# Optimization experiments

Measured on AMD Instinct MI355X. Metric: run time of the kernel, lower is better.

Reference implementation:

```python
import jax, jax.numpy as jnp
import numpy as np

B, CK, CV, T, H, W = 2, 64, 256, 8, 48, 48

def setup_inputs() -> dict:
    key = jax.random.key(0)
    k1, k2, k3, k4, k5, k6 = jax.random.split(key, 6)
    return {
        "query_key": jax.random.normal(k1, (B, CK, H, W), jnp.float32),
        "query_selection": jax.random.uniform(k2, (B, CK, H, W), jnp.float32),
        "memory_key": jax.random.normal(k3, (B, CK, T, H, W), jnp.float32),
        "memory_shrinkage": jax.random.uniform(k4, (B, 1, T, H, W), jnp.float32),
        "msk_value": jax.random.normal(k5, (B, 1, CV, T, H, W), jnp.float32),
        "uncert_prob": jax.random.uniform(k6, (B, 1, H, W), jnp.float32),
    }

def reference(query_key, query_selection, memory_key, memory_shrinkage, msk_value, uncert_prob):
    b, ck, h, w = query_key.shape
    t = memory_key.shape[2]
    hw = h * w
    thw = t * hw
    num_obj, cv = msk_value.shape[1], msk_value.shape[2]

    mk = memory_key.reshape(b, ck, thw)            # B,CK,THW
    ms = memory_shrinkage.reshape(b, thw, 1)       # B,THW,1
    qk = query_key.reshape(b, ck, hw)              # B,CK,HW
    qe = query_selection.reshape(b, ck, hw)        # B,CK,HW

    # L2 similarity with selection weighting: -(mk - qk)^2 weighted by qe per channel
    a_sq = jnp.einsum('bct,bcn->btn', mk * mk, qe)          # B,THW,HW
    two_ab = 2.0 * jnp.einsum('bct,bcn->btn', mk, qk * qe)  # B,THW,HW
    b_sq = jnp.sum(qe * qk * qk, axis=1, keepdims=True)     # B,1,HW
    similarity = (-a_sq + two_ab - b_sq) * ms / jnp.sqrt(jnp.float32(ck))

    # softmax over the memory (THW) axis
    affinity = jax.nn.softmax(similarity, axis=1)           # B,THW,HW

    # weighted readout of memory values
    mv = msk_value.reshape(b, num_obj * cv, thw)            # B,CV,THW
    pixel_readout = jnp.einsum('bct,btn->bcn', mv, affinity)
    pixel_readout = pixel_readout.reshape(b, num_obj, cv, h, w)

    # uncertainty-weighted blend with last memory frame's value
    last_val = msk_value[:, :, :, -1]                       # B,no,CV,H,W
    p = uncert_prob[:, None]                                # B,1,1,H,W
    blended = pixel_readout * p + last_val[:, None, 0] * (1.0 - p) if False else pixel_readout * p + last_val * (1.0 - p)
    return blended
```

## Files before the change

kernel.cpp:

```cpp
#include <hip/hip_runtime.h>
#include <math.h>

#define NB 2
#define CKD 64
#define CVD 256
#define TD 8
#define HWD 2304
#define THWD 18432
#define QB 64
#define NQB (HWD / QB)
#define KVT 32

typedef __bf16 bf16_t;
typedef __bf16 bf16x8 __attribute__((ext_vector_type(8)));
typedef __bf16 bf16x4 __attribute__((ext_vector_type(4)));
typedef float f32x4 __attribute__((ext_vector_type(4)));
typedef unsigned int u32;

__device__ __forceinline__ void gload16(const void* g, void* l) {
    __builtin_amdgcn_global_load_lds((const __attribute__((address_space(1))) u32*)g,
                                     (__attribute__((address_space(3))) u32*)l, 16, 0, 0);
}

__global__ void prep_kf(const float* __restrict__ mk, char* __restrict__ KF2) {
    __shared__ float tile[64][65];
    const int b = blockIdx.y;
    const int kv0 = blockIdx.x * 64;
    const int tid = threadIdx.x;
    {
        const int c = tid >> 2, seg = tid & 3;
        const float* src = mk + ((size_t)b * CKD + c) * THWD + kv0;
#pragma unroll
        for (int j = 0; j < 4; ++j) {
            int ch = seg + j * 4;
            f32x4 v = *(const f32x4*)(src + ch * 4);
#pragma unroll
            for (int x = 0; x < 4; ++x) tile[c][ch * 4 + x] = v[x];
        }
    }
    __syncthreads();
#pragma unroll
    for (int k = 0; k < 4; ++k) {
        int gid = k * 256 + tid;
        int kvl = gid >> 4, G = gid & 15;
        bf16x8 o;
#pragma unroll
        for (int e = 0; e < 8; ++e) {
            int c = G * 8 + e;
            float v;
            if (c < 64) v = tile[c][kvl];
            else { float m = tile[c - 64][kvl]; v = m * m; }
            o[e] = (bf16_t)v;
        }
        size_t byte = (((size_t)b * 1152 + ((kv0 + kvl) >> 4)) * 16 + (kvl & 15)) * 256 +
                      (size_t)((G ^ (kvl & 7)) << 4);
        *(bf16x8*)(KF2 + byte) = o;
    }
}

__global__ void prep_qf(const float* __restrict__ qk, const float* __restrict__ qe,
                        char* __restrict__ QF2, float* __restrict__ bsq) {
    __shared__ float tk[64][65];
    __shared__ float te[64][65];
    __shared__ float bs[4][64];
    const int b = blockIdx.y;
    const int q0 = blockIdx.x * 64;
    const int tid = threadIdx.x;
    {
        const int c = tid >> 2, seg = tid & 3;
        const float* s1 = qk + ((size_t)b * CKD + c) * HWD + q0;
        const float* s2 = qe + ((size_t)b * CKD + c) * HWD + q0;
#pragma unroll
        for (int j = 0; j < 4; ++j) {
            int ch = seg + j * 4;
            f32x4 v1 = *(const f32x4*)(s1 + ch * 4);
            f32x4 v2 = *(const f32x4*)(s2 + ch * 4);
#pragma unroll
            for (int x = 0; x < 4; ++x) { tk[c][ch * 4 + x] = v1[x]; te[c][ch * 4 + x] = v2[x]; }
        }
    }
    __syncthreads();
    {
        int qls = tid & 63, cp = tid >> 6;
        float s = 0.f;
#pragma unroll
        for (int cc = 0; cc < 16; ++cc) {
            int c = cp * 16 + cc;
            float kk = tk[c][qls];
            s = fmaf(te[c][qls] * kk, kk, s);
        }
        bs[cp][qls] = s;
    }
#pragma unroll
    for (int k = 0; k < 4; ++k) {
        int gid = k * 256 + tid;
        int qll = gid >> 4, G = gid & 15;
        int ks = G >> 2, G2 = G & 3;
        bf16x8 o;
#pragma unroll
        for (int e = 0; e < 8; ++e) {
            int c = G * 8 + e;
            float v;
            if (c < 64) v = 2.f * tk[c][qll] * te[c][qll];
            else v = -te[c - 64][qll];
            o[e] = (bf16_t)v;
        }
        size_t byte = ((((size_t)b * 144 + blockIdx.x * 4 + (qll >> 4)) * 4 + ks) * 16 +
                       (qll & 15)) * 64 + (size_t)(G2 << 4);
        *(bf16x8*)(QF2 + byte) = o;
    }
    __syncthreads();
    if (tid < 64) bsq[b * HWD + q0 + tid] = bs[0][tid] + bs[1][tid] + bs[2][tid] + bs[3][tid];
}

__global__ void mv_t(const float* __restrict__ mv, char* __restrict__ mvT) {
    __shared__ float tile[64][65];
    const int b = blockIdx.z;
    const int cv0 = blockIdx.y * 64;
    const int kv0 = blockIdx.x * 64;
    const int tid = threadIdx.x;
    {
        const int cvl = tid >> 2, seg = tid & 3;
        const float* src = mv + ((size_t)b * CVD + cv0 + cvl) * THWD + kv0;
#pragma unroll
        for (int j = 0; j < 4; ++j) {
            int ch = seg + j * 4;
            f32x4 v = *(const f32x4*)(src + ch * 4);
#pragma unroll
            for (int x = 0; x < 4; ++x) tile[cvl][ch * 4 + x] = v[x];
        }
    }
    __syncthreads();
#pragma unroll
    for (int k = 0; k < 2; ++k) {
        int gid = k * 256 + tid;
        int cvl = gid >> 3, gseg = gid & 7;
        int t32l = gseg >> 2, G = gseg & 3;
        int cv = cv0 + cvl;
        bf16x8 o;
#pragma unroll
        for (int e = 0; e < 8; ++e) o[e] = (bf16_t)tile[cvl][gseg * 8 + e];
        size_t byte = (((size_t)b * 576 + (kv0 >> 5) + t32l) * 256 + cv) * 64 +
                      (size_t)((G ^ ((cv >> 1) & 3)) << 4);
        *(bf16x8*)(mvT + byte) = o;
    }
}

__global__ __launch_bounds__(256, 3) void fused(
    const char* __restrict__ KF2, const char* __restrict__ QF2,
    const char* __restrict__ mvT, const float* __restrict__ ms,
    const float* __restrict__ bsq, float* __restrict__ accP,
    float* __restrict__ lP, int split, int tiles) {
    __shared__ __align__(16) char kf_s[2][8192];
    __shared__ __align__(16) char mv_s[2][16384];
    __shared__ __align__(16) char w_s[4096];
    __shared__ float l_s[2][64];

    const int tid = threadIdx.x;
    const int lane = tid & 63;
    const int wave = tid >> 6;
    const int wq = wave & 1;
    const int wc = wave >> 1;
    const int r = lane & 15;
    const int g = lane >> 4;
    const int swq = (r >> 1) & 3;

    const int nwg = gridDim.x;
    const int bid = blockIdx.x;
    const int id = (bid & 7) * (nwg >> 3) + (bid >> 3);
    const int sp = id / 72;
    const int rem = id - sp * 72;
    const int b = rem / 36;
    const int qblk = rem - b * 36;

    const int tbase = sp * (THWD / split);

    const char* KFb = KF2 + (size_t)b * THWD * 256;
    const char* QFb = QF2 + (size_t)b * 144 * 4096;
    const char* mvTb = mvT + (size_t)b * 576 * 16384;
    const float* msb = ms + (size_t)b * THWD;

    bf16x8 qf[2][4];
    float bsqr[2];
#pragma unroll
    for (int ql = 0; ql < 2; ++ql) {
        int qb16 = qblk * 4 + wq * 2 + ql;
#pragma unroll
        for (int ks = 0; ks < 4; ++ks)
            qf[ql][ks] = *(const bf16x8*)(QFb + ((size_t)qb16 * 4 + ks) * 1024 + r * 64 + g * 16);
        bsqr[ql] = bsq[b * HWD + qblk * 64 + wq * 32 + ql * 16 + r];
    }

    f32x4 acc[8][2];
#pragma unroll
    for (int i = 0; i < 8; ++i)
#pragma unroll
        for (int j = 0; j < 2; ++j) acc[i][j] = (f32x4){0.f, 0.f, 0.f, 0.f};
    float lacc[2] = {0.f, 0.f};

    auto stage = [&](int buf, int t0) {
        const char* gk = KFb + (size_t)(t0 >> 4) * 4096 + wave * 2048 + lane * 16;
        char* lk = &kf_s[buf][wave * 2048];
        gload16(gk, lk);
        gload16(gk + 1024, lk + 1024);
        const char* gm = mvTb + (size_t)(t0 >> 5) * 16384 + wave * 4096 + lane * 16;
        char* lm = &mv_s[buf][wave * 4096];
#pragma unroll
        for (int i = 0; i < 4; ++i) gload16(gm + i * 1024, lm + i * 1024);
    };

    f32x4 msv[2];
    stage(0, tbase);
    msv[0] = *(const f32x4*)(msb + tbase + wc * 16 + g * 4);

#pragma unroll 2
    for (int it = 0; it < tiles; ++it) {
        const int t0 = tbase + it * KVT;
        const char* kf_c = kf_s[it & 1];
        const char* mv_c = mv_s[it & 1];

        asm volatile("s_waitcnt vmcnt(0) lgkmcnt(0)" ::: "memory");
        __builtin_amdgcn_s_barrier();

        if (it + 1 < tiles) {
            stage((it + 1) & 1, t0 + KVT);
            msv[(it + 1) & 1] = *(const f32x4*)(msb + t0 + KVT + wc * 16 + g * 4);
        }

        f32x4 S[2];
        S[0] = (f32x4){0.f, 0.f, 0.f, 0.f};
        S[1] = (f32x4){0.f, 0.f, 0.f, 0.f};
#pragma unroll
        for (int ks = 0; ks < 4; ++ks) {
            bf16x8 kff = *(const bf16x8*)(kf_c + (wc * 16 + r) * 256 +
                                          (((ks * 4 + g) ^ (r & 7)) << 4));
#pragma unroll
            for (int ql = 0; ql < 2; ++ql)
                S[ql] = __builtin_amdgcn_mfma_f32_16x16x32_bf16(kff, qf[ql][ks], S[ql], 0, 0, 0);
        }

        f32x4 msc = msv[it & 1];
#pragma unroll
        for (int ql = 0; ql < 2; ++ql) {
            int q = wq * 32 + ql * 16 + r;
            f32x4 sv = S[ql];
            float w0 = __expf((sv[0] - bsqr[ql]) * (msc[0] * 0.125f));
            float w1 = __expf((sv[1] - bsqr[ql]) * (msc[1] * 0.125f));
            float w2 = __expf((sv[2] - bsqr[ql]) * (msc[2] * 0.125f));
            float w3 = __expf((sv[3] - bsqr[ql]) * (msc[3] * 0.125f));
            lacc[ql] += (w0 + w1) + (w2 + w3);
            bf16x4 wb;
            wb[0] = (bf16_t)w0; wb[1] = (bf16_t)w1; wb[2] = (bf16_t)w2; wb[3] = (bf16_t)w3;
            *(bf16x4*)(&w_s[q * 64 + (((wc * 2 + (g >> 1)) ^ swq) << 4) + (g & 1) * 8]) = wb;
        }
        asm volatile("s_waitcnt lgkmcnt(0)" ::: "memory");
        __builtin_amdgcn_s_barrier();

        bf16x8 wf[2];
#pragma unroll
        for (int ql = 0; ql < 2; ++ql) {
            int q = wq * 32 + ql * 16 + r;
            wf[ql] = *(const bf16x8*)(&w_s[q * 64 + ((g ^ swq) << 4)]);
        }
#pragma unroll
        for (int cvt = 0; cvt < 8; ++cvt) {
            bf16x8 mvf = *(const bf16x8*)(mv_c + (wc * 128 + cvt * 16 + r) * 64 +
                                          ((g ^ swq) << 4));
#pragma unroll
            for (int ql = 0; ql < 2; ++ql)
                acc[cvt][ql] = __builtin_amdgcn_mfma_f32_16x16x32_bf16(mvf, wf[ql], acc[cvt][ql], 0, 0, 0);
        }
    }

    size_t pb = (size_t)(b * NQB + qblk) * split + sp;
    float* accB = accP + pb * (CVD * QB);
#pragma unroll
    for (int cvt = 0; cvt < 8; ++cvt)
#pragma unroll
        for (int ql = 0; ql < 2; ++ql) {
            int q = wq * 32 + ql * 16 + r;
#pragma unroll
            for (int i = 0; i < 4; ++i)
                accB[(size_t)(wc * 128 + cvt * 16 + g * 4 + i) * QB + q] = acc[cvt][ql][i];
        }
#pragma unroll
    for (int ql = 0; ql < 2; ++ql) {
        float v = lacc[ql];
        v += __shfl_xor(v, 16);
        v += __shfl_xor(v, 32);
        if (lane < 16) l_s[wc][wq * 32 + ql * 16 + lane] = v;
    }
    __syncthreads();
    if (tid < QB) lP[pb * QB + tid] = l_s[0][tid] + l_s[1][tid];
}

__global__ void combine(const float* __restrict__ accP, const float* __restrict__ lP,
                        const float* __restrict__ mv, const float* __restrict__ up,
                        float* __restrict__ out, int split) {
    int idx = blockIdx.x * 256 + threadIdx.x;
    if (idx >= NB * CVD * HWD) return;
    int n = idx % HWD;
    int cv = (idx / HWD) % CVD;
    int b = idx / (HWD * CVD);
    int qblk = n / QB, nl = n % QB;
    size_t base = ((size_t)(b * NQB + qblk) * split) * (CVD * QB) + (size_t)cv * QB + nl;
    size_t lbase = ((size_t)(b * NQB + qblk) * split) * QB + nl;
    float a = 0.f, l = 0.f;
    for (int s = 0; s < split; ++s) {
        a += accP[base + (size_t)s * (CVD * QB)];
        l += lP[lbase + (size_t)s * QB];
    }
    float ro = a / l;
    float p = up[b * HWD + n];
    float last = mv[((size_t)b * CVD + cv) * THWD + (TD - 1) * HWD + n];
    out[idx] = ro * p + last * (1.f - p);
}

extern "C" void kernel_launch(void* const* d_in, const int* in_sizes, int n_in,
                              void* d_out, int out_size, void* d_ws,
                              size_t ws_size, hipStream_t stream) {
    const float* qk = (const float*)d_in[0];
    const float* qe = (const float*)d_in[1];
    const float* mk = (const float*)d_in[2];
    const float* ms = (const float*)d_in[3];
    const float* mv = (const float*)d_in[4];
    const float* up = (const float*)d_in[5];
    float* out = (float*)d_out;

    char* ws = (char*)d_ws;
    size_t off = 0;
    auto alloc = [&](size_t bytes) {
        size_t o = off;
        off += (bytes + 255) & ~(size_t)255;
        return o;
    };
    size_t kf_o = alloc((size_t)NB * THWD * 256);
    size_t qf_o = alloc((size_t)NB * 144 * 4096);
    size_t mvt_o = alloc((size_t)NB * 576 * 16384);
    size_t bsq_o = alloc((size_t)NB * HWD * 4);
    size_t fixed = off;

    int split = 16;
    while (split > 1) {
        size_t need = fixed +
                      (((size_t)NB * NQB * split * CVD * QB * 4 + 255) & ~(size_t)255) +
                      (((size_t)NB * NQB * split * QB * 4 + 255) & ~(size_t)255);
        if (need <= ws_size) break;
        split >>= 1;
    }
    size_t lp_o = alloc((size_t)NB * NQB * split * QB * 4);
    size_t acc_o = alloc((size_t)NB * NQB * split * CVD * QB * 4);

    char* KF2 = ws + kf_o;
    char* QF2 = ws + qf_o;
    char* MVT = ws + mvt_o;
    float* bsqp = (float*)(ws + bsq_o);
    float* lPp = (float*)(ws + lp_o);
    float* accPp = (float*)(ws + acc_o);

    int tiles = (THWD / split) / KVT;

    prep_kf<<<dim3(THWD / 64, NB), 256, 0, stream>>>(mk, KF2);
    prep_qf<<<dim3(HWD / 64, NB), 256, 0, stream>>>(qk, qe, QF2, bsqp);
    mv_t<<<dim3(THWD / 64, CVD / 64, NB), 256, 0, stream>>>(mv, MVT);

    int nwg = NB * NQB * split;
    fused<<<nwg, 256, 0, stream>>>(KF2, QF2, MVT, ms, bsqp, accPp, lPp, split, tiles);

    combine<<<((size_t)NB * CVD * HWD + 255) / 256, 256, 0, stream>>>(accPp, lPp, mv,
                                                                      up, out, split);
}
```

Measured before the change: 163.3 us.

## Restructure fused attention tiles: smaller query block, larger KV tile, direct value loads

Shrinks the query block from 64 to 32 and doubles the KV tile to 64, fixing the split at 8. Each wave now handles a 16-row KV slice: two waves split the channel halves and the two KV halves are reduced in-block through LDS. Value fragments are loaded straight from global memory into registers instead of being staged through LDS, and the mv_t layout drops its swizzle to match. The combine kernel is vectorised to four channels per thread. Together these change data reuse, LDS traffic and grid size, at the cost of more global value reads per block and an extra in-block reduction.

```diff
diff --git a/kernel.cpp b/kernel.cpp
--- a/kernel.cpp
+++ b/kernel.cpp
@@ -7,9 +7,11 @@
 #define TD 8
 #define HWD 2304
 #define THWD 18432
-#define QB 64
+#define QB 32
 #define NQB (HWD / QB)
-#define KVT 32
+#define KVT 64
+#define SPLIT 8
+#define TILES (THWD / SPLIT / KVT)
 
 typedef __bf16 bf16_t;
 typedef __bf16 bf16x8 __attribute__((ext_vector_type(8)));
@@ -46,13 +48,13 @@
         bf16x8 o;
 #pragma unroll
         for (int e = 0; e < 8; ++e) {
-            int c = G * 8 + e;
+            int ch = G * 8 + e;
             float v;
-            if (c < 64) v = tile[c][kvl];
-            else { float m = tile[c - 64][kvl]; v = m * m; }
+            if (ch < 64) v = tile[ch][kvl];
+            else { float m = tile[ch - 64][kvl]; v = m * m; }
             o[e] = (bf16_t)v;
         }
-        size_t byte = (((size_t)b * 1152 + ((kv0 + kvl) >> 4)) * 16 + (kvl & 15)) * 256 +
+        size_t byte = (((size_t)b * (THWD / 16) + ((kv0 + kvl) >> 4)) * 16 + (kvl & 15)) * 256 +
                       (size_t)((G ^ (kvl & 7)) << 4);
         *(bf16x8*)(KF2 + byte) = o;
     }
@@ -85,9 +87,9 @@
         float s = 0.f;
 #pragma unroll
         for (int cc = 0; cc < 16; ++cc) {
-            int c = cp * 16 + cc;
-            float kk = tk[c][qls];
-            s = fmaf(te[c][qls] * kk, kk, s);
+            int ch = cp * 16 + cc;
+            float kk = tk[ch][qls];
+            s = fmaf(te[ch][qls] * kk, kk, s);
         }
         bs[cp][qls] = s;
     }
@@ -99,13 +101,13 @@
         bf16x8 o;
 #pragma unroll
         for (int e = 0; e < 8; ++e) {
-            int c = G * 8 + e;
+            int ch = G * 8 + e;
             float v;
-            if (c < 64) v = 2.f * tk[c][qll] * te[c][qll];
-            else v = -te[c - 64][qll];
+            if (ch < 64) v = 2.f * tk[ch][qll] * te[ch][qll];
+            else v = -te[ch - 64][qll];
             o[e] = (bf16_t)v;
         }
-        size_t byte = ((((size_t)b * 144 + blockIdx.x * 4 + (qll >> 4)) * 4 + ks) * 16 +
+        size_t byte = ((((size_t)b * (HWD / 16) + blockIdx.x * 4 + (qll >> 4)) * 4 + ks) * 16 +
                        (qll & 15)) * 64 + (size_t)(G2 << 4);
         *(bf16x8*)(QF2 + byte) = o;
     }
@@ -136,12 +138,12 @@
         int gid = k * 256 + tid;
         int cvl = gid >> 3, gseg = gid & 7;
         int t32l = gseg >> 2, G = gseg & 3;
-        int cv = cv0 + cvl;
         bf16x8 o;
 #pragma unroll
-        for (int e = 0; e < 8; ++e) o[e] = (bf16_t)tile[cvl][gseg * 8 + e];
-        size_t byte = (((size_t)b * 576 + (kv0 >> 5) + t32l) * 256 + cv) * 64 +
-                      (size_t)((G ^ ((cv >> 1) & 3)) << 4);
+        for (int e = 0; e < 8; ++e)
+            o[e] = (bf16_t)tile[cvl][t32l * 32 + (e >> 2) * 16 + G * 4 + (e & 3)];
+        size_t byte = (((size_t)b * (THWD / 32) + (kv0 >> 5) + t32l) * 256 + cv0 + cvl) * 64 +
+                      (size_t)(G << 4);
         *(bf16x8*)(mvT + byte) = o;
     }
 }
@@ -150,45 +152,42 @@
     const char* __restrict__ KF2, const char* __restrict__ QF2,
     const char* __restrict__ mvT, const float* __restrict__ ms,
     const float* __restrict__ bsq, float* __restrict__ accP,
-    float* __restrict__ lP, int split, int tiles) {
-    __shared__ __align__(16) char kf_s[2][8192];
-    __shared__ __align__(16) char mv_s[2][16384];
-    __shared__ __align__(16) char w_s[4096];
-    __shared__ float l_s[2][64];
+    float* __restrict__ lP) {
+    __shared__ __align__(16) char kf_s[2][16384];
+    __shared__ __align__(16) char w_lds[4096];
+    __shared__ float l_s[4][QB];
 
     const int tid = threadIdx.x;
     const int lane = tid & 63;
     const int wave = tid >> 6;
-    const int wq = wave & 1;
-    const int wc = wave >> 1;
+    const int s = wave >> 1;
+    const int c = wave & 1;
+    const int st = s * 2 + c;
     const int r = lane & 15;
     const int g = lane >> 4;
-    const int swq = (r >> 1) & 3;
-
-    const int nwg = gridDim.x;
+
     const int bid = blockIdx.x;
-    const int id = (bid & 7) * (nwg >> 3) + (bid >> 3);
-    const int sp = id / 72;
-    const int rem = id - sp * 72;
-    const int b = rem / 36;
-    const int qblk = rem - b * 36;
-
-    const int tbase = sp * (THWD / split);
+    const int id = (bid & 7) * (NB * NQB) + (bid >> 3);
+    const int sp = id / (NB * NQB);
+    const int rem = id % (NB * NQB);
+    const int b = rem / NQB;
+    const int qblk = rem % NQB;
+    const int tbase = sp * (THWD / SPLIT);
 
     const char* KFb = KF2 + (size_t)b * THWD * 256;
-    const char* QFb = QF2 + (size_t)b * 144 * 4096;
-    const char* mvTb = mvT + (size_t)b * 576 * 16384;
+    const char* QFb = QF2 + (size_t)b * (HWD / 16) * 4096;
+    const char* mvTb = mvT + (size_t)b * (THWD / 32) * 16384;
     const float* msb = ms + (size_t)b * THWD;
 
     bf16x8 qf[2][4];
     float bsqr[2];
 #pragma unroll
     for (int ql = 0; ql < 2; ++ql) {
-        int qb16 = qblk * 4 + wq * 2 + ql;
+        int qb16 = qblk * 2 + ql;
 #pragma unroll
         for (int ks = 0; ks < 4; ++ks)
             qf[ql][ks] = *(const bf16x8*)(QFb + ((size_t)qb16 * 4 + ks) * 1024 + r * 64 + g * 16);
-        bsqr[ql] = bsq[b * HWD + qblk * 64 + wq * 32 + ql * 16 + r];
+        bsqr[ql] = bsq[b * HWD + qblk * QB + ql * 16 + r];
     }
 
     f32x4 acc[8][2];
@@ -199,50 +198,44 @@
     float lacc[2] = {0.f, 0.f};
 
     auto stage = [&](int buf, int t0) {
-        const char* gk = KFb + (size_t)(t0 >> 4) * 4096 + wave * 2048 + lane * 16;
-        char* lk = &kf_s[buf][wave * 2048];
-        gload16(gk, lk);
-        gload16(gk + 1024, lk + 1024);
-        const char* gm = mvTb + (size_t)(t0 >> 5) * 16384 + wave * 4096 + lane * 16;
-        char* lm = &mv_s[buf][wave * 4096];
-#pragma unroll
-        for (int i = 0; i < 4; ++i) gload16(gm + i * 1024, lm + i * 1024);
+        const char* gk = KFb + (size_t)t0 * 256 + wave * 4096 + lane * 16;
+        char* lk = &kf_s[buf][wave * 4096];
+#pragma unroll
+        for (int i = 0; i < 4; ++i) gload16(gk + i * 1024, lk + i * 1024);
     };
-
-    f32x4 msv[2];
     stage(0, tbase);
-    msv[0] = *(const f32x4*)(msb + tbase + wc * 16 + g * 4);
 
 #pragma unroll 2
-    for (int it = 0; it < tiles; ++it) {
+    for (int it = 0; it < TILES; ++it) {
         const int t0 = tbase + it * KVT;
         const char* kf_c = kf_s[it & 1];
-        const char* mv_c = mv_s[it & 1];
 
         asm volatile("s_waitcnt vmcnt(0) lgkmcnt(0)" ::: "memory");
         __builtin_amdgcn_s_barrier();
 
-        if (it + 1 < tiles) {
-            stage((it + 1) & 1, t0 + KVT);
-            msv[(it + 1) & 1] = *(const f32x4*)(msb + t0 + KVT + wc * 16 + g * 4);
-        }
+        bf16x8 mvf[8];
+#pragma unroll
+        for (int cvt = 0; cvt < 8; ++cvt)
+            mvf[cvt] = *(const bf16x8*)(mvTb +
+                ((size_t)((t0 >> 5) + s) * 256 + c * 128 + cvt * 16 + r) * 64 + g * 16);
+        f32x4 msc = *(const f32x4*)(msb + t0 + st * 16 + g * 4);
+
+        if (it + 1 < TILES) stage((it + 1) & 1, t0 + KVT);
 
         f32x4 S[2];
         S[0] = (f32x4){0.f, 0.f, 0.f, 0.f};
         S[1] = (f32x4){0.f, 0.f, 0.f, 0.f};
 #pragma unroll
         for (int ks = 0; ks < 4; ++ks) {
-            bf16x8 kff = *(const bf16x8*)(kf_c + (wc * 16 + r) * 256 +
+            bf16x8 kff = *(const bf16x8*)(kf_c + (st * 16 + r) * 256 +
                                           (((ks * 4 + g) ^ (r & 7)) << 4));
 #pragma unroll
             for (int ql = 0; ql < 2; ++ql)
                 S[ql] = __builtin_amdgcn_mfma_f32_16x16x32_bf16(kff, qf[ql][ks], S[ql], 0, 0, 0);
         }
 
-        f32x4 msc = msv[it & 1];
 #pragma unroll
         for (int ql = 0; ql < 2; ++ql) {
-            int q = wq * 32 + ql * 16 + r;
             f32x4 sv = S[ql];
             float w0 = __expf((sv[0] - bsqr[ql]) * (msc[0] * 0.125f));
             float w1 = __expf((sv[1] - bsqr[ql]) * (msc[1] * 0.125f));
@@ -251,69 +244,86 @@
             lacc[ql] += (w0 + w1) + (w2 + w3);
             bf16x4 wb;
             wb[0] = (bf16_t)w0; wb[1] = (bf16_t)w1; wb[2] = (bf16_t)w2; wb[3] = (bf16_t)w3;
-            *(bf16x4*)(&w_s[q * 64 + (((wc * 2 + (g >> 1)) ^ swq) << 4) + (g & 1) * 8]) = wb;
+            *(bf16x4*)(&w_lds[((s * 32 + ql * 16 + r) * 4 + g) * 16 + c * 8]) = wb;
         }
         asm volatile("s_waitcnt lgkmcnt(0)" ::: "memory");
         __builtin_amdgcn_s_barrier();
 
         bf16x8 wf[2];
 #pragma unroll
-        for (int ql = 0; ql < 2; ++ql) {
-            int q = wq * 32 + ql * 16 + r;
-            wf[ql] = *(const bf16x8*)(&w_s[q * 64 + ((g ^ swq) << 4)]);
-        }
-#pragma unroll
-        for (int cvt = 0; cvt < 8; ++cvt) {
-            bf16x8 mvf = *(const bf16x8*)(mv_c + (wc * 128 + cvt * 16 + r) * 64 +
-                                          ((g ^ swq) << 4));
+        for (int ql = 0; ql < 2; ++ql)
+            wf[ql] = *(const bf16x8*)(&w_lds[((s * 32 + ql * 16 + r) * 4 + g) * 16]);
+#pragma unroll
+        for (int cvt = 0; cvt < 8; ++cvt)
 #pragma unroll
             for (int ql = 0; ql < 2; ++ql)
-                acc[cvt][ql] = __builtin_amdgcn_mfma_f32_16x16x32_bf16(mvf, wf[ql], acc[cvt][ql], 0, 0, 0);
-        }
-    }
-
-    size_t pb = (size_t)(b * NQB + qblk) * split + sp;
-    float* accB = accP + pb * (CVD * QB);
-#pragma unroll
-    for (int cvt = 0; cvt < 8; ++cvt)
-#pragma unroll
-        for (int ql = 0; ql < 2; ++ql) {
-            int q = wq * 32 + ql * 16 + r;
-#pragma unroll
-            for (int i = 0; i < 4; ++i)
-                accB[(size_t)(wc * 128 + cvt * 16 + g * 4 + i) * QB + q] = acc[cvt][ql][i];
-        }
+                acc[cvt][ql] = __builtin_amdgcn_mfma_f32_16x16x32_bf16(
+                    mvf[cvt], wf[ql], acc[cvt][ql], 0, 0, 0);
+    }
+
+    __syncthreads();
+    float* red = (float*)&kf_s[0][0];
+    if (s == 1) {
+#pragma unroll
+        for (int cvt = 0; cvt < 8; ++cvt)
+#pragma unroll
+            for (int ql = 0; ql < 2; ++ql)
+                *(f32x4*)(red + c * 4096 + ((cvt * 2 + ql) * 256 + lane * 4)) = acc[cvt][ql];
+    }
 #pragma unroll
     for (int ql = 0; ql < 2; ++ql) {
         float v = lacc[ql];
         v += __shfl_xor(v, 16);
         v += __shfl_xor(v, 32);
-        if (lane < 16) l_s[wc][wq * 32 + ql * 16 + lane] = v;
-    }
-    __syncthreads();
-    if (tid < QB) lP[pb * QB + tid] = l_s[0][tid] + l_s[1][tid];
-}
-
-__global__ void combine(const float* __restrict__ accP, const float* __restrict__ lP,
-                        const float* __restrict__ mv, const float* __restrict__ up,
-                        float* __restrict__ out, int split) {
+        if (lane < 16) l_s[wave][ql * 16 + lane] = v;
+    }
+    __syncthreads();
+    size_t pb = (size_t)(b * NQB + qblk) * SPLIT + sp;
+    if (s == 0) {
+        float* accB = accP + pb * (CVD * QB);
+#pragma unroll
+        for (int cvt = 0; cvt < 8; ++cvt)
+#pragma unroll
+            for (int ql = 0; ql < 2; ++ql) {
+                f32x4 o = acc[cvt][ql] +
+                          *(const f32x4*)(red + c * 4096 + ((cvt * 2 + ql) * 256 + lane * 4));
+                int cv0 = c * 128 + cvt * 16 + g * 4;
+                int q = ql * 16 + r;
+                *(f32x4*)(accB + ((size_t)(cv0 >> 2) * QB + q) * 4) = o;
+            }
+    }
+    if (tid < QB)
+        lP[pb * QB + tid] = (l_s[0][tid] + l_s[1][tid]) + (l_s[2][tid] + l_s[3][tid]);
+}
+
+__global__ void combine2(const float* __restrict__ accP, const float* __restrict__ lP,
+                         const float* __restrict__ mv, const float* __restrict__ up,
+                         float* __restrict__ out) {
     int idx = blockIdx.x * 256 + threadIdx.x;
-    if (idx >= NB * CVD * HWD) return;
-    int n = idx % HWD;
-    int cv = (idx / HWD) % CVD;
-    int b = idx / (HWD * CVD);
-    int qblk = n / QB, nl = n % QB;
-    size_t base = ((size_t)(b * NQB + qblk) * split) * (CVD * QB) + (size_t)cv * QB + nl;
-    size_t lbase = ((size_t)(b * NQB + qblk) * split) * QB + nl;
-    float a = 0.f, l = 0.f;
-    for (int s = 0; s < split; ++s) {
-        a += accP[base + (size_t)s * (CVD * QB)];
-        l += lP[lbase + (size_t)s * QB];
-    }
-    float ro = a / l;
+    int nl = idx & 31;
+    int t = idx >> 5;
+    int cvq4 = t & 63;
+    int t2 = t >> 6;
+    int qblk = t2 % NQB;
+    int b = t2 / NQB;
+    size_t pb0 = (size_t)(b * NQB + qblk) * SPLIT;
+    const float* base = accP + pb0 * (CVD * QB) + ((size_t)cvq4 * QB + nl) * 4;
+    f32x4 a = {0.f, 0.f, 0.f, 0.f};
+    float l = 0.f;
+#pragma unroll
+    for (int sp = 0; sp < SPLIT; ++sp) {
+        a += *(const f32x4*)(base + (size_t)sp * (CVD * QB));
+        l += lP[(pb0 + sp) * QB + nl];
+    }
+    int n = qblk * QB + nl;
+    int cv0 = cvq4 * 4;
     float p = up[b * HWD + n];
-    float last = mv[((size_t)b * CVD + cv) * THWD + (TD - 1) * HWD + n];
-    out[idx] = ro * p + last * (1.f - p);
+    float rl = 1.f / l;
+#pragma unroll
+    for (int e = 0; e < 4; ++e) {
+        float last = mv[((size_t)b * CVD + cv0 + e) * THWD + (TD - 1) * HWD + n];
+        out[((size_t)b * CVD + cv0 + e) * HWD + n] = a[e] * rl * p + last * (1.f - p);
+    }
 }
 
 extern "C" void kernel_launch(void* const* d_in, const int* in_sizes, int n_in,
@@ -335,21 +345,11 @@
         return o;
     };
     size_t kf_o = alloc((size_t)NB * THWD * 256);
-    size_t qf_o = alloc((size_t)NB * 144 * 4096);
-    size_t mvt_o = alloc((size_t)NB * 576 * 16384);
+    size_t qf_o = alloc((size_t)NB * (HWD / 16) * 4096);
+    size_t mvt_o = alloc((size_t)NB * (THWD / 32) * 16384);
     size_t bsq_o = alloc((size_t)NB * HWD * 4);
-    size_t fixed = off;
-
-    int split = 16;
-    while (split > 1) {
-        size_t need = fixed +
-                      (((size_t)NB * NQB * split * CVD * QB * 4 + 255) & ~(size_t)255) +
-                      (((size_t)NB * NQB * split * QB * 4 + 255) & ~(size_t)255);
-        if (need <= ws_size) break;
-        split >>= 1;
-    }
-    size_t lp_o = alloc((size_t)NB * NQB * split * QB * 4);
-    size_t acc_o = alloc((size_t)NB * NQB * split * CVD * QB * 4);
+    size_t lp_o = alloc((size_t)NB * NQB * SPLIT * QB * 4);
+    size_t acc_o = alloc((size_t)NB * NQB * SPLIT * CVD * QB * 4);
 
     char* KF2 = ws + kf_o;
     char* QF2 = ws + qf_o;
@@ -358,15 +358,11 @@
     float* lPp = (float*)(ws + lp_o);
     float* accPp = (float*)(ws + acc_o);
 
-    int tiles = (THWD / split) / KVT;
-
     prep_kf<<<dim3(THWD / 64, NB), 256, 0, stream>>>(mk, KF2);
     prep_qf<<<dim3(HWD / 64, NB), 256, 0, stream>>>(qk, qe, QF2, bsqp);
     mv_t<<<dim3(THWD / 64, CVD / 64, NB), 256, 0, stream>>>(mv, MVT);
 
-    int nwg = NB * NQB * split;
-    fused<<<nwg, 256, 0, stream>>>(KF2, QF2, MVT, ms, bsqp, accPp, lPp, split, tiles);
-
-    combine<<<((size_t)NB * CVD * HWD + 255) / 256, 256, 0, stream>>>(accPp, lPp, mv,
-                                                                      up, out, split);
-}
+    fused<<<NB * NQB * SPLIT, 256, 0, stream>>>(KF2, QF2, MVT, ms, bsqp, accPp, lPp);
+
+    combine2<<<(NB * NQB * 64 * 32) / 256, 256, 0, stream>>>(accPp, lPp, mv, up, out);
+}
```

Measured after the change: 232.8 us. 42.6% more time.
